# Kernel tuning notes

Hardware: AMD Instinct MI355X
Metric: run time of the kernel (lower is better)

Reference implementation:

```python
import jax, jax.numpy as jnp
import numpy as np

N = 100000
E = 3200000
VOCAB = 100000
FEAT = 128
HID = 16
NUM_CLASSES = 20
EPS = 1e-12


def setup_inputs() -> dict:
    key = jax.random.key(0)
    ks = jax.random.split(key, 8)
    x_ids = jax.random.randint(ks[0], (N, 1), 0, VOCAB)
    # edges guaranteed non-self (PyG AGNNConv removes self-loops then re-adds)
    dst = jax.random.randint(ks[1], (E,), 0, N)
    off = jax.random.randint(ks[2], (E,), 1, N)
    src = (dst + off) % N
    edge_index = jnp.stack([src, dst], axis=0)
    emb = jax.random.normal(ks[3], (VOCAB, FEAT), dtype=jnp.float32)
    W1 = jax.random.normal(ks[4], (FEAT, HID), dtype=jnp.float32) / np.sqrt(FEAT)
    b1 = jnp.zeros((HID,), dtype=jnp.float32)
    beta2 = jnp.ones((), dtype=jnp.float32)  # learnable beta of prop2
    W2 = jax.random.normal(ks[5], (HID, NUM_CLASSES), dtype=jnp.float32) / np.sqrt(HID)
    b2 = jnp.zeros((NUM_CLASSES,), dtype=jnp.float32)
    return {"x_ids": x_ids, "edge_index": edge_index, "emb": emb,
            "W1": W1, "b1": b1, "beta2": beta2, "W2": W2, "b2": b2}


def agnn_prop(x, src, dst, beta):
    # AGNNConv: P_ij = softmax_j( beta * cos(x_i, x_j) ); out_i = sum_j P_ij x_j
    n = x.shape[0]
    xn = x / jnp.maximum(jnp.linalg.norm(x, axis=-1, keepdims=True), EPS)
    alpha = beta * jnp.sum(xn[dst] * xn[src], axis=-1)          # [E']
    m = jax.ops.segment_max(alpha, dst, num_segments=n)          # per-target max
    e = jnp.exp(alpha - m[dst])
    s = jax.ops.segment_sum(e, dst, num_segments=n)
    w = e / s[dst]                                               # edge softmax weights
    return jax.ops.segment_sum(w[:, None] * x[src], dst, num_segments=n)


def reference(x_ids, edge_index, emb, W1, b1, beta2, W2, b2):
    # add self-loops (PyG AGNNConv default)
    loop = jnp.arange(N)
    src = jnp.concatenate([edge_index[0], loop])
    dst = jnp.concatenate([edge_index[1], loop])

    x = emb[x_ids.squeeze(-1)]                 # [N, FEAT]
    # dropout is identity in eval mode
    x = jax.nn.relu(x @ W1 + b1)               # [N, 16]
    x = agnn_prop(x, src, dst, jnp.float32(1.0))  # prop1: fixed beta=1
    x = agnn_prop(x, src, dst, beta2)             # prop2: learnable beta
    x = x @ W2 + b2                             # [N, num_classes]
    return jax.nn.log_softmax(x, axis=1)
```

## Files before the change

kernel.cpp:

```cpp
#include <hip/hip_runtime.h>
#include <math.h>

#define NN    100000
#define NE    3200000
#define FEAT  128
#define HID   16
#define NCLS  20
#define NBKT  391
#define NBLKC 512
#define TB    1024
#define CHNK  ((NE + NBLKC - 1) / NBLKC)
#define KC_SL 7
#define KD_SL 9

typedef _Float16 hf;
typedef _Float16 hf2 __attribute__((ext_vector_type(2)));

__device__ __forceinline__ float dot2f(hf2 a, hf2 b) {
#if defined(__has_builtin) && __has_builtin(__builtin_amdgcn_fdot2)
  return __builtin_amdgcn_fdot2(a, b, 0.0f, false);
#else
  return fmaf((float)a.y, (float)b.y, (float)a.x * (float)b.x);
#endif
}

__global__ __launch_bounds__(256) void k_embed_mlp(
    const int* __restrict__ ids, const float* __restrict__ emb,
    const float* __restrict__ W1, const float* __restrict__ b1,
    hf* __restrict__ hx, float* __restrict__ invn) {
  __shared__ float sW[FEAT * HID];
  __shared__ float sx[16][FEAT + 4];
  for (int i = threadIdx.x; i < FEAT * HID; i += 256) sW[i] = W1[i];
  int node = blockIdx.x * 16 + (threadIdx.x >> 4);
  int nl = threadIdx.x >> 4;
  int k = threadIdx.x & 15;
  const float4* er = (const float4*)(emb + (size_t)ids[node] * FEAT);
  float4 ra = er[2 * k], rb = er[2 * k + 1];
  *(float4*)&sx[nl][8 * k] = ra;
  *(float4*)&sx[nl][8 * k + 4] = rb;
  __syncthreads();
  float acc = b1[k];
  const float* xr = sx[nl];
#pragma unroll
  for (int j = 0; j < FEAT; ++j) acc = fmaf(xr[j], sW[j * HID + k], acc);
  acc = fmaxf(acc, 0.0f);
  hf h = (hf)acc;
  float a = (float)h;
  float n2 = a * a;
  n2 += __shfl_xor(n2, 1); n2 += __shfl_xor(n2, 2);
  n2 += __shfl_xor(n2, 4); n2 += __shfl_xor(n2, 8);
  hx[node * HID + k] = h;
  if (k == 0) invn[node] = rsqrtf(fmaxf(n2, 1e-24f));
}

__global__ __launch_bounds__(256) void k_zero(int* __restrict__ c, int n) {
  int i = blockIdx.x * 256 + threadIdx.x;
  if (i < n) c[i] = 0;
}

__global__ __launch_bounds__(TB) void kA(
    const int* __restrict__ edst, int* __restrict__ gcount) {
  __shared__ int h[NBKT];
  for (int i = threadIdx.x; i < NBKT; i += TB) h[i] = 0;
  __syncthreads();
  int s0 = blockIdx.x * CHNK, s1 = min(NE, s0 + CHNK);
  for (int i = s0 + threadIdx.x; i < s1; i += TB)
    atomicAdd(&h[__builtin_nontemporal_load(edst + i) >> 8], 1);
  __syncthreads();
  for (int i = threadIdx.x; i < NBKT; i += TB)
    if (h[i]) atomicAdd(&gcount[i], h[i]);
}

__global__ __launch_bounds__(512) void kB(
    const int* __restrict__ gcount, int* __restrict__ gbase,
    int* __restrict__ gcur, int* __restrict__ rowptr) {
  __shared__ int sd[512];
  int tid = threadIdx.x;
  int v = (tid < NBKT) ? gcount[tid] : 0;
  sd[tid] = v;
  __syncthreads();
  for (int off = 1; off < 512; off <<= 1) {
    int t = (tid >= off) ? sd[tid - off] : 0;
    __syncthreads();
    sd[tid] += t;
    __syncthreads();
  }
  if (tid < NBKT) { int b = sd[tid] - v; gbase[tid] = b; gcur[tid] = b; }
  if (tid == 0) rowptr[NN] = NE;
}

__global__ __launch_bounds__(TB) void kC(
    const int* __restrict__ esrc, const int* __restrict__ edst,
    int* __restrict__ gcur, unsigned* __restrict__ strm) {
  __shared__ int h[NBKT];
  __shared__ int lofs[NBKT + 1];
  __shared__ int basel[NBKT];
  __shared__ int sd[512];
  __shared__ unsigned lsort[CHNK];
  int tid = threadIdx.x;
  for (int i = tid; i < NBKT; i += TB) h[i] = 0;
  __syncthreads();
  int s0 = blockIdx.x * CHNK, s1 = min(NE, s0 + CHNK);
  int total = s1 - s0;
  int dc[KC_SL], sc[KC_SL];
#pragma unroll
  for (int j = 0; j < KC_SL; ++j) {
    int i = s0 + tid + j * TB;
    if (i < s1) {
      int d = __builtin_nontemporal_load(edst + i);
      dc[j] = d;
      sc[j] = __builtin_nontemporal_load(esrc + i);
      atomicAdd(&h[d >> 8], 1);
    }
  }
  __syncthreads();
  int v = (tid < NBKT) ? h[tid] : 0;
  if (tid < 512) sd[tid] = v;
  __syncthreads();
  for (int off = 1; off < 512; off <<= 1) {
    int t = (tid < 512 && tid >= off) ? sd[tid - off] : 0;
    __syncthreads();
    if (tid < 512) sd[tid] += t;
    __syncthreads();
  }
  if (tid < NBKT) {
    lofs[tid] = sd[tid] - v;
    basel[tid] = v ? atomicAdd(&gcur[tid], v) : 0;
  }
  if (tid == 0) lofs[NBKT] = total;
  __syncthreads();
  for (int i = tid; i < NBKT; i += TB) h[i] = 0;
  __syncthreads();
#pragma unroll
  for (int j = 0; j < KC_SL; ++j) {
    int i = s0 + tid + j * TB;
    if (i < s1) {
      int d = dc[j];
      int b = d >> 8;
      int p = lofs[b] + atomicAdd(&h[b], 1);
      lsort[p] = (unsigned)sc[j] | ((unsigned)(d & 255) << 17);
    }
  }
  __syncthreads();
  for (int j = tid; j < total; j += TB) {
    int lo = 0, hi = NBKT;
    while (hi - lo > 1) {
      int mid = (lo + hi) >> 1;
      if (lofs[mid] <= j) lo = mid; else hi = mid;
    }
    strm[basel[lo] + (j - lofs[lo])] = lsort[j];
  }
}

__global__ __launch_bounds__(TB) void kD(
    const int* __restrict__ gcount, const int* __restrict__ gbase,
    const unsigned* __restrict__ strm, int* __restrict__ rowptr,
    int* __restrict__ col) {
  __shared__ int cnt[256];
  __shared__ int cur[256];
  __shared__ int sd[256];
  int b = blockIdx.x, tid = threadIdx.x;
  int base = gbase[b], n = gcount[b];
  if (tid < 256) cnt[tid] = 0;
  __syncthreads();
  unsigned wc[KD_SL];
#pragma unroll
  for (int j = 0; j < KD_SL; ++j) {
    int i = tid + j * TB;
    if (i < n) {
      unsigned w = strm[base + i];
      wc[j] = w;
      atomicAdd(&cnt[w >> 17], 1);
    }
  }
  for (int i = tid + KD_SL * TB; i < n; i += TB)
    atomicAdd(&cnt[strm[base + i] >> 17], 1);
  __syncthreads();
  int v = (tid < 256) ? cnt[tid] : 0;
  if (tid < 256) sd[tid] = v;
  __syncthreads();
  for (int off = 1; off < 256; off <<= 1) {
    int t = (tid >= off && tid < 256) ? sd[tid - off] : 0;
    __syncthreads();
    if (tid < 256) sd[tid] += t;
    __syncthreads();
  }
  if (tid < 256) {
    int excl = sd[tid] - v;
    cur[tid] = excl;
    int node = (b << 8) + tid;
    if (node < NN) rowptr[node] = base + excl;
  }
  __syncthreads();
#pragma unroll
  for (int j = 0; j < KD_SL; ++j) {
    int i = tid + j * TB;
    if (i < n) {
      unsigned w = wc[j];
      int p = atomicAdd(&cur[w >> 17], 1);
      col[base + p] = (int)(w & 0x1FFFFu);
    }
  }
  for (int i = tid + KD_SL * TB; i < n; i += TB) {
    unsigned w = strm[base + i];
    int p = atomicAdd(&cur[w >> 17], 1);
    col[base + p] = (int)(w & 0x1FFFFu);
  }
}

#define PROP_COMPUTE4(c0, c1, c2, c3, j0, j1, j2, j3)                        \
  {                                                                          \
    float r0 = dot2f(xdn2, c0);                                              \
    float r1 = dot2f(xdn2, c1);                                              \
    float r2 = dot2f(xdn2, c2);                                              \
    float r3 = dot2f(xdn2, c3);                                              \
    r0 += __shfl_xor(r0, 1); r1 += __shfl_xor(r1, 1);                        \
    r2 += __shfl_xor(r2, 1); r3 += __shfl_xor(r3, 1);                        \
    r0 += __shfl_xor(r0, 2); r1 += __shfl_xor(r1, 2);                        \
    r2 += __shfl_xor(r2, 2); r3 += __shfl_xor(r3, 2);                        \
    r0 += __shfl_xor(r0, 4); r1 += __shfl_xor(r1, 4);                        \
    r2 += __shfl_xor(r2, 4); r3 += __shfl_xor(r3, 4);                        \
    float e0 = __expf(beta * r0 * j0);                                       \
    float e1 = __expf(beta * r1 * j1);                                       \
    float e2v = __expf(beta * r2 * j2);                                      \
    float e3 = __expf(beta * r3 * j3);                                       \
    s += (e0 + e1) + (e2v + e3);                                             \
    a0 = fmaf(e0, (float)c0.x, a0);  a1 = fmaf(e0, (float)c0.y, a1);         \
    a0 = fmaf(e1, (float)c1.x, a0);  a1 = fmaf(e1, (float)c1.y, a1);         \
    a0 = fmaf(e2v, (float)c2.x, a0); a1 = fmaf(e2v, (float)c2.y, a1);        \
    a0 = fmaf(e3, (float)c3.x, a0);  a1 = fmaf(e3, (float)c3.y, a1);         \
  }

#define PROP_LOAD8(base_e)                                                   \
  {                                                                          \
    int u0 = col[(base_e)];     int u1 = col[(base_e) + 1];                  \
    int u2 = col[(base_e) + 2]; int u3 = col[(base_e) + 3];                  \
    int u4 = col[(base_e) + 4]; int u5 = col[(base_e) + 5];                  \
    int u6 = col[(base_e) + 6]; int u7 = col[(base_e) + 7];                  \
    f0 = H[u0 * 8 + l]; f1 = H[u1 * 8 + l];                                  \
    f2 = H[u2 * 8 + l]; f3 = H[u3 * 8 + l];                                  \
    f4 = H[u4 * 8 + l]; f5 = H[u5 * 8 + l];                                  \
    f6 = H[u6 * 8 + l]; f7 = H[u7 * 8 + l];                                  \
    i0 = invn[u0]; i1 = invn[u1]; i2 = invn[u2]; i3 = invn[u3];              \
    i4 = invn[u4]; i5 = invn[u5]; i6 = invn[u6]; i7 = invn[u7];              \
  }

__global__ __launch_bounds__(256) void k_prop(
    const int* __restrict__ rowptr, const int* __restrict__ col,
    const hf* __restrict__ hx, const float* __restrict__ invn,
    const float* __restrict__ beta_p,
    hf* __restrict__ hxo, float* __restrict__ invno) {
  int node = blockIdx.x * 32 + (threadIdx.x >> 3);
  int l = threadIdx.x & 7;
  if (node >= NN) return;
  float beta = beta_p ? beta_p[0] : 1.0f;
  const hf2* H = (const hf2*)hx;
  hf2 xi2 = H[node * 8 + l];
  float x0 = (float)xi2.x, x1 = (float)xi2.y;
  float invi = invn[node];
  float n2 = x0 * x0 + x1 * x1;
  n2 += __shfl_xor(n2, 1); n2 += __shfl_xor(n2, 2); n2 += __shfl_xor(n2, 4);
  hf2 xdn2; xdn2.x = (hf)(x0 * invi); xdn2.y = (hf)(x1 * invi);
  float dself = n2 * invi * invi;
  float es = __expf(beta * dself);
  float s = es;
  float a0 = es * x0, a1 = es * x1;
  int e = rowptr[node], e2 = rowptr[node + 1];
  hf2 f0, f1, f2, f3, f4, f5, f6, f7;
  float i0, i1, i2, i3, i4, i5, i6, i7;
  if (e + 8 <= e2) PROP_LOAD8(e);
  for (; e + 16 <= e2; e += 8) {
    hf2 c0 = f0, c1 = f1, c2 = f2, c3 = f3, c4 = f4, c5 = f5, c6 = f6, c7 = f7;
    float j0 = i0, j1 = i1, j2 = i2, j3 = i3, j4 = i4, j5 = i5, j6 = i6, j7 = i7;
    PROP_LOAD8(e + 8);
    PROP_COMPUTE4(c0, c1, c2, c3, j0, j1, j2, j3);
    PROP_COMPUTE4(c4, c5, c6, c7, j4, j5, j6, j7);
  }
  if (e + 8 <= e2) {
    PROP_COMPUTE4(f0, f1, f2, f3, i0, i1, i2, i3);
    PROP_COMPUTE4(f4, f5, f6, f7, i4, i5, i6, i7);
    e += 8;
  }
  if (e + 4 <= e2) {
    int u0 = col[e], u1 = col[e + 1], u2 = col[e + 2], u3 = col[e + 3];
    hf2 c0 = H[u0 * 8 + l], c1 = H[u1 * 8 + l];
    hf2 c2 = H[u2 * 8 + l], c3 = H[u3 * 8 + l];
    float j0 = invn[u0], j1 = invn[u1], j2 = invn[u2], j3 = invn[u3];
    PROP_COMPUTE4(c0, c1, c2, c3, j0, j1, j2, j3);
    e += 4;
  }
  for (; e < e2; ++e) {
    int u = col[e];
    hf2 b = H[u * 8 + l];
    float r = dot2f(xdn2, b);
    r += __shfl_xor(r, 1); r += __shfl_xor(r, 2); r += __shfl_xor(r, 4);
    float ee = __expf(beta * r * invn[u]);
    s += ee;
    a0 = fmaf(ee, (float)b.x, a0); a1 = fmaf(ee, (float)b.y, a1);
  }
  float inv_s = 1.0f / s;
  hf2 o; o.x = (hf)(a0 * inv_s); o.y = (hf)(a1 * inv_s);
  float g0 = (float)o.x, g1 = (float)o.y;
  float m2 = g0 * g0 + g1 * g1;
  m2 += __shfl_xor(m2, 1); m2 += __shfl_xor(m2, 2); m2 += __shfl_xor(m2, 4);
  ((hf2*)hxo)[node * 8 + l] = o;
  if (l == 0) invno[node] = rsqrtf(fmaxf(m2, 1e-24f));
}

__global__ __launch_bounds__(256) void k_cls(
    const hf* __restrict__ x, const float* __restrict__ W2,
    const float* __restrict__ b2, float* __restrict__ out) {
  __shared__ float sW[HID * NCLS];
  __shared__ float sb[NCLS];
  for (int i = threadIdx.x; i < HID * NCLS; i += 256) sW[i] = W2[i];
  if (threadIdx.x < NCLS) sb[threadIdx.x] = b2[threadIdx.x];
  __syncthreads();
  int i = blockIdx.x * 256 + threadIdx.x;
  if (i >= NN) return;
  float xi[HID];
  const hf2* X = (const hf2*)(x + (size_t)i * HID);
#pragma unroll
  for (int r = 0; r < 8; ++r) {
    hf2 v = X[r];
    xi[2 * r] = (float)v.x; xi[2 * r + 1] = (float)v.y;
  }
  float logit[NCLS];
  float mx = -1e30f;
#pragma unroll
  for (int c = 0; c < NCLS; ++c) {
    float acc = sb[c];
#pragma unroll
    for (int kk = 0; kk < HID; ++kk) acc = fmaf(xi[kk], sW[kk * NCLS + c], acc);
    logit[c] = acc;
    mx = fmaxf(mx, acc);
  }
  float ssum = 0.0f;
#pragma unroll
  for (int c = 0; c < NCLS; ++c) ssum += __expf(logit[c] - mx);
  float lse = mx + logf(ssum);
  float* o = out + (size_t)i * NCLS;
#pragma unroll
  for (int c = 0; c < NCLS; ++c) o[c] = logit[c] - lse;
}

extern "C" void kernel_launch(void* const* d_in, const int* in_sizes, int n_in,
                              void* d_out, int out_size, void* d_ws, size_t ws_size,
                              hipStream_t stream) {
  const int*   x_ids = (const int*)d_in[0];
  const int*   ei    = (const int*)d_in[1];
  const float* emb   = (const float*)d_in[2];
  const float* W1    = (const float*)d_in[3];
  const float* b1    = (const float*)d_in[4];
  const float* beta2 = (const float*)d_in[5];
  const float* W2    = (const float*)d_in[6];
  const float* b2    = (const float*)d_in[7];
  float* out = (float*)d_out;

  unsigned* strm = (unsigned*)d_ws;
  int* col    = (int*)d_ws + NE;
  int* rowptr = col + NE;
  int* gcount = rowptr + (NN + 1);
  int* gbase  = gcount + NBKT;
  int* gcur   = gbase + NBKT;
  hf*    hx0   = (hf*)d_ws;
  hf*    hx1   = hx0 + (size_t)NN * HID;
  float* invn0 = (float*)(hx1 + (size_t)NN * HID);
  float* invn1 = invn0 + NN;

  const int* esrc = ei;
  const int* edst = ei + NE;

  const int gN = (NN + 255) / 256;
  const int gM = (NN + 15) / 16;
  const int gP = (NN + 31) / 32;

  k_zero<<<2, 256, 0, stream>>>(gcount, NBKT);
  kA<<<NBLKC, TB, 0, stream>>>(edst, gcount);
  kB<<<1, 512, 0, stream>>>(gcount, gbase, gcur, rowptr);
  kC<<<NBLKC, TB, 0, stream>>>(esrc, edst, gcur, strm);
  kD<<<NBKT, TB, 0, stream>>>(gcount, gbase, strm, rowptr, col);

  k_embed_mlp<<<gM, 256, 0, stream>>>(x_ids, emb, W1, b1, hx0, invn0);

  k_prop<<<gP, 256, 0, stream>>>(rowptr, col, hx0, invn0, nullptr, hx1, invn1);
  k_prop<<<gP, 256, 0, stream>>>(rowptr, col, hx1, invn1, beta2, hx0, invn0);

  k_cls<<<gN, 256, 0, stream>>>(hx0, W2, b2, out);
}
```

Measured before the change: 192.3 us.

## Sort nodes by degree via counting sort to balance prop wavefronts

Adds three small kernels that build a degree histogram, scan it, and scatter node ids into degree-sorted order. Both propagation kernels then map each 8-lane group to a node taken from this order, so wavefronts process nodes of similar degree. The goal is to cut lane divergence and tail imbalance in the per-edge loop. The cost is three extra launches, one extra indirection per node, and less locality in the node-feature reads and output writes.

```diff
diff --git a/kernel.cpp b/kernel.cpp
--- a/kernel.cpp
+++ b/kernel.cpp
@@ -12,6 +12,7 @@
 #define CHNK  ((NE + NBLKC - 1) / NBLKC)
 #define KC_SL 7
 #define KD_SL 9
+#define NSB   98
 
 typedef _Float16 hf;
 typedef _Float16 hf2 __attribute__((ext_vector_type(2)));
@@ -205,6 +206,65 @@
     unsigned w = strm[base + i];
     int p = atomicAdd(&cur[w >> 17], 1);
     col[base + p] = (int)(w & 0x1FFFFu);
+  }
+}
+
+__global__ __launch_bounds__(1024) void kS1(
+    const int* __restrict__ rowptr, int* __restrict__ dhist) {
+  __shared__ int h[256];
+  int tid = threadIdx.x;
+  if (tid < 256) h[tid] = 0;
+  __syncthreads();
+  int node = blockIdx.x * 1024 + tid;
+  if (node < NN) {
+    int deg = rowptr[node + 1] - rowptr[node];
+    atomicAdd(&h[min(deg, 255)], 1);
+  }
+  __syncthreads();
+  if (tid < 256 && h[tid]) atomicAdd(&dhist[tid], h[tid]);
+}
+
+__global__ __launch_bounds__(256) void kS2(
+    const int* __restrict__ dhist, int* __restrict__ dcur) {
+  __shared__ int sd[256];
+  int tid = threadIdx.x;
+  int v = dhist[tid];
+  sd[tid] = v;
+  __syncthreads();
+  for (int off = 1; off < 256; off <<= 1) {
+    int t = (tid >= off) ? sd[tid - off] : 0;
+    __syncthreads();
+    sd[tid] += t;
+    __syncthreads();
+  }
+  dcur[tid] = sd[tid] - v;
+}
+
+__global__ __launch_bounds__(1024) void kS3(
+    const int* __restrict__ rowptr, int* __restrict__ dcur,
+    int* __restrict__ nodeord) {
+  __shared__ int h[256];
+  __shared__ int basel[256];
+  int tid = threadIdx.x;
+  if (tid < 256) h[tid] = 0;
+  __syncthreads();
+  int node = blockIdx.x * 1024 + tid;
+  int bin = -1;
+  if (node < NN) {
+    int deg = rowptr[node + 1] - rowptr[node];
+    bin = min(deg, 255);
+    atomicAdd(&h[bin], 1);
+  }
+  __syncthreads();
+  if (tid < 256) {
+    int c = h[tid];
+    basel[tid] = c ? atomicAdd(&dcur[tid], c) : 0;
+    h[tid] = 0;
+  }
+  __syncthreads();
+  if (node < NN) {
+    int off = atomicAdd(&h[bin], 1);
+    nodeord[basel[bin] + off] = node;
   }
 }
 
@@ -246,13 +306,15 @@
   }
 
 __global__ __launch_bounds__(256) void k_prop(
+    const int* __restrict__ nodeord,
     const int* __restrict__ rowptr, const int* __restrict__ col,
     const hf* __restrict__ hx, const float* __restrict__ invn,
     const float* __restrict__ beta_p,
     hf* __restrict__ hxo, float* __restrict__ invno) {
-  int node = blockIdx.x * 32 + (threadIdx.x >> 3);
+  int gid = blockIdx.x * 32 + (threadIdx.x >> 3);
   int l = threadIdx.x & 7;
-  if (node >= NN) return;
+  if (gid >= NN) return;
+  int node = nodeord[gid];
   float beta = beta_p ? beta_p[0] : 1.0f;
   const hf2* H = (const hf2*)hx;
   hf2 xi2 = H[node * 8 + l];
@@ -362,10 +424,13 @@
   int* gcount = rowptr + (NN + 1);
   int* gbase  = gcount + NBKT;
   int* gcur   = gbase + NBKT;
+  int* dhist  = gcur + NBKT;
+  int* dcur   = dhist + 256;
   hf*    hx0   = (hf*)d_ws;
   hf*    hx1   = hx0 + (size_t)NN * HID;
   float* invn0 = (float*)(hx1 + (size_t)NN * HID);
   float* invn1 = invn0 + NN;
+  int*   nodeord = (int*)(invn1 + NN);
 
   const int* esrc = ei;
   const int* edst = ei + NE;
@@ -375,15 +440,20 @@
   const int gP = (NN + 31) / 32;
 
   k_zero<<<2, 256, 0, stream>>>(gcount, NBKT);
+  k_zero<<<1, 256, 0, stream>>>(dhist, 256);
   kA<<<NBLKC, TB, 0, stream>>>(edst, gcount);
   kB<<<1, 512, 0, stream>>>(gcount, gbase, gcur, rowptr);
   kC<<<NBLKC, TB, 0, stream>>>(esrc, edst, gcur, strm);
   kD<<<NBKT, TB, 0, stream>>>(gcount, gbase, strm, rowptr, col);
 
+  kS1<<<NSB, 1024, 0, stream>>>(rowptr, dhist);
+  kS2<<<1, 256, 0, stream>>>(dhist, dcur);
+  kS3<<<NSB, 1024, 0, stream>>>(rowptr, dcur, nodeord);
+
   k_embed_mlp<<<gM, 256, 0, stream>>>(x_ids, emb, W1, b1, hx0, invn0);
 
-  k_prop<<<gP, 256, 0, stream>>>(rowptr, col, hx0, invn0, nullptr, hx1, invn1);
-  k_prop<<<gP, 256, 0, stream>>>(rowptr, col, hx1, invn1, beta2, hx0, invn0);
+  k_prop<<<gP, 256, 0, stream>>>(nodeord, rowptr, col, hx0, invn0, nullptr, hx1, invn1);
+  k_prop<<<gP, 256, 0, stream>>>(nodeord, rowptr, col, hx1, invn1, beta2, hx0, invn0);
 
   k_cls<<<gN, 256, 0, stream>>>(hx0, W2, b2, out);
 }
```

New measurement: 209.2 us. +8.8%, slower.
